# Optimization experiments

Hardware: AMD Instinct MI355X
Metric: run time of the kernel (lower is better)

Reference implementation:

```python
import jax, jax.numpy as jnp
import numpy as np

N, E, G, T = 4096, 16384, 128, 100
DIMS = [(5, 64), (64, 128), (128, 256)]
EPS = 1e-5


def setup_inputs() -> dict:
    key = jax.random.key(0)
    ks = iter(jax.random.split(key, 64))
    d = {}
    d["x"] = jax.random.normal(next(ks), (N, 5), jnp.float32)
    d["edge_index"] = jax.random.randint(next(ks), (2, E), 0, N, jnp.int64)
    d["edge_attr"] = jax.random.uniform(next(ks), (E, 3), jnp.float32)
    d["batch_seg"] = jnp.sort(jax.random.randint(next(ks), (N,), 0, G, jnp.int64))
    for l, (cin, cout) in enumerate(DIMS, start=1):
        d[f"l{l}_W1"] = jax.random.normal(next(ks), (3, 32), jnp.float32) * 0.3
        d[f"l{l}_b1"] = jnp.zeros((32,), jnp.float32)
        d[f"l{l}_W2"] = jax.random.normal(next(ks), (32, cin * cout), jnp.float32) * 0.05
        d[f"l{l}_b2"] = jnp.zeros((cin * cout,), jnp.float32)
        d[f"l{l}_root"] = jax.random.normal(next(ks), (cin, cout), jnp.float32) * 0.1
        d[f"l{l}_bias"] = jnp.zeros((cout,), jnp.float32)
        d[f"bn{l}_g"] = jnp.ones((cout,), jnp.float32)
        d[f"bn{l}_b"] = jnp.zeros((cout,), jnp.float32)
        d[f"bn{l}_m"] = jax.random.normal(next(ks), (cout,), jnp.float32) * 0.01
        d[f"bn{l}_v"] = jax.random.uniform(next(ks), (cout,), jnp.float32, 0.5, 1.5)
    d["mlp_W"] = jax.random.normal(next(ks), (256, T), jnp.float32) * 0.06
    d["mlp_b"] = jnp.zeros((T,), jnp.float32)
    return d


def _nnconv(h, src, dst, edge_attr, W1, b1, W2, b2, root, bias, cin, cout):
    # edge MLP -> per-edge weight matrix [E, cin, cout]
    ew = (jax.nn.relu(edge_attr @ W1 + b1) @ W2 + b2).reshape(-1, cin, cout)
    msg = jnp.einsum('ei,eio->eo', h[src], ew)  # gather + per-edge matmul
    ssum = jax.ops.segment_sum(msg, dst, num_segments=N)
    cnt = jax.ops.segment_sum(jnp.ones((msg.shape[0],), msg.dtype), dst, num_segments=N)
    agg = ssum / jnp.maximum(cnt, 1.0)[:, None]  # scatter-mean
    return h @ root + agg + bias


def _bn(h, g, b, m, v):
    return g * (h - m) * jax.lax.rsqrt(v + EPS) + b


def reference(x, edge_index, edge_attr, batch_seg,
              l1_W1, l1_b1, l1_W2, l1_b2, l1_root, l1_bias, bn1_g, bn1_b, bn1_m, bn1_v,
              l2_W1, l2_b1, l2_W2, l2_b2, l2_root, l2_bias, bn2_g, bn2_b, bn2_m, bn2_v,
              l3_W1, l3_b1, l3_W2, l3_b2, l3_root, l3_bias, bn3_g, bn3_b, bn3_m, bn3_v,
              mlp_W, mlp_b):
    src, dst = edge_index[0], edge_index[1]
    h = _nnconv(x, src, dst, edge_attr, l1_W1, l1_b1, l1_W2, l1_b2, l1_root, l1_bias, 5, 64)
    h = jax.nn.relu(_bn(h, bn1_g, bn1_b, bn1_m, bn1_v))
    h = _nnconv(h, src, dst, edge_attr, l2_W1, l2_b1, l2_W2, l2_b2, l2_root, l2_bias, 64, 128)
    h = jax.nn.relu(_bn(h, bn2_g, bn2_b, bn2_m, bn2_v))
    h = _nnconv(h, src, dst, edge_attr, l3_W1, l3_b1, l3_W2, l3_b2, l3_root, l3_bias, 128, 256)
    h = jax.nn.relu(_bn(h, bn3_g, bn3_b, bn3_m, bn3_v))
    # global mean pool over graphs
    psum = jax.ops.segment_sum(h, batch_seg, num_segments=G)
    pcnt = jax.ops.segment_sum(jnp.ones((N,), h.dtype), batch_seg, num_segments=G)
    pooled = psum / jnp.maximum(pcnt, 1.0)[:, None]
    out = pooled @ mlp_W + mlp_b
    return jnp.where(out > 0, out, 0.1 * out)  # LeakyReLU(0.1)
```

## Files before the change

### kernel.cpp

```cpp
#include <hip/hip_runtime.h>
#include <cstdint>
#include <cstddef>

#define BN_EPS 1e-5f

typedef short bf16x8 __attribute__((ext_vector_type(8)));
typedef float f32x4  __attribute__((ext_vector_type(4)));
typedef unsigned short u16x8 __attribute__((ext_vector_type(8)));

__device__ __forceinline__ uint16_t f2bf_rte(float f) {
  uint32_t u = __float_as_uint(f);
  uint32_t r = u + 0x7fffu + ((u >> 16) & 1u);
  return (uint16_t)(r >> 16);
}
__device__ __forceinline__ float bf2f(uint16_t h) {
  return __uint_as_float(((uint32_t)h) << 16);
}
__device__ __forceinline__ void split_bf(float v, uint16_t& hi, uint16_t& lo) {
  hi = f2bf_rte(v);
  lo = f2bf_rte(v - bf2f(hi));
}

__global__ void hist_k(const int* __restrict__ dst, int* __restrict__ cnt, int E) {
  int e = blockIdx.x * blockDim.x + threadIdx.x;
  if (e < E) atomicAdd(&cnt[dst[e]], 1);
}

__global__ __launch_bounds__(1024) void scan_k(const int* __restrict__ cnt,
                                               int* __restrict__ offsets,
                                               int* __restrict__ cursor,
                                               int N, int total) {
  __shared__ int part[1024];
  int t = threadIdx.x;
  int a0 = cnt[4*t+0], a1 = cnt[4*t+1], a2 = cnt[4*t+2], a3 = cnt[4*t+3];
  part[t] = a0 + a1 + a2 + a3;
  __syncthreads();
  for (int off = 1; off < 1024; off <<= 1) {
    int v = (t >= off) ? part[t - off] : 0;
    __syncthreads();
    part[t] += v;
    __syncthreads();
  }
  int excl = (t == 0) ? 0 : part[t-1];
  int o0 = excl, o1 = o0 + a0, o2 = o1 + a1, o3 = o2 + a2;
  offsets[4*t+0] = o0; offsets[4*t+1] = o1; offsets[4*t+2] = o2; offsets[4*t+3] = o3;
  cursor [4*t+0] = o0; cursor [4*t+1] = o1; cursor [4*t+2] = o2; cursor [4*t+3] = o3;
  if (t == 0) offsets[N] = total;
}

__global__ void scatter_k(const int* __restrict__ dst, int* __restrict__ cursor,
                          int* __restrict__ csr, int E) {
  int e = blockIdx.x * blockDim.x + threadIdx.x;
  if (e < E) {
    int d = dst[e];
    int pos = atomicAdd(&cursor[d], 1);
    csr[pos] = e;
  }
}

__device__ __forceinline__ void w2pt_one(int idx, const float* W2, const float* b2,
                                         const float* root, uint16_t* Bhi, uint16_t* Blo,
                                         int cin, int cout, int Kpad) {
  int o  = idx / Kpad;
  int ki = idx - o * Kpad;
  float v = 0.f;
  if (ki < 34 * cin) {
    int k = ki / cin;
    int i = ki - k * cin;
    if (k < 32)       v = W2[(size_t)k * cin * cout + (size_t)i * cout + o];
    else if (k == 32) v = b2[(size_t)i * cout + o];
    else              v = root[(size_t)i * cout + o];
  }
  uint16_t hi, lo;
  split_bf(v, hi, lo);
  Bhi[idx] = hi;
  Blo[idx] = lo;
}

__global__ void build_W2pT_all_k(const float* W2a, const float* b2a, const float* roota,
                                 uint16_t* Bhia, uint16_t* Bloa,
                                 const float* W2b, const float* b2b, const float* rootb,
                                 uint16_t* Bhib, uint16_t* Blob,
                                 const float* W2c, const float* b2c, const float* rootc,
                                 uint16_t* Bhic, uint16_t* Bloc) {
  const int T1 = 64 * 192, T2 = 128 * 2176, T3 = 256 * 4352;
  int idx = blockIdx.x * blockDim.x + threadIdx.x;
  if (idx < T1) {
    w2pt_one(idx, W2a, b2a, roota, Bhia, Bloa, 5, 64, 192);
  } else if (idx < T1 + T2) {
    w2pt_one(idx - T1, W2b, b2b, rootb, Bhib, Blob, 64, 128, 2176);
  } else if (idx < T1 + T2 + T3) {
    w2pt_one(idx - T1 - T2, W2c, b2c, rootc, Bhic, Bloc, 128, 256, 4352);
  }
}

template<int CIN>
__global__ __launch_bounds__(256) void build_S_vec_k(const float* __restrict__ Craw,
                                                     const float* __restrict__ pbias,
                                                     const float* __restrict__ pg,
                                                     const float* __restrict__ pb,
                                                     const float* __restrict__ pm,
                                                     const float* __restrict__ pv,
                                                     const float* __restrict__ ea,
                                                     const float* __restrict__ W1,
                                                     const float* __restrict__ b1,
                                                     const int* __restrict__ src,
                                                     const int* __restrict__ csr,
                                                     const int* __restrict__ offsets,
                                                     uint16_t* __restrict__ Shi,
                                                     uint16_t* __restrict__ Slo,
                                                     int Kpad) {
  constexpr int CH = 8;
  constexpr int K1 = 33 * CIN;
  constexpr int NCH = K1 / 8;
  constexpr int NP = (NCH + 255) / 256;
  __shared__ float hs[CH][CIN];
  __shared__ float zs[CH][33];
  __shared__ int   es[CH];
  __shared__ float sA[CIN], tA[CIN];
  const int n = blockIdx.x;
  const int tid = threadIdx.x;
  if (tid < CIN) {
    float s = pg[tid] * rsqrtf(pv[tid] + BN_EPS);
    sA[tid] = s;
    tA[tid] = (pbias[tid] - pm[tid]) * s + pb[tid];
  }
  const int base = offsets[n];
  const int deg  = offsets[n+1] - base;
  const float scale = 1.f / fmaxf((float)deg, 1.f);
  float acc[NP][8];
#pragma unroll
  for (int p = 0; p < NP; p++)
#pragma unroll
    for (int j = 0; j < 8; j++) acc[p][j] = 0.f;

  for (int c0 = 0; c0 < deg; c0 += CH) {
    const int cc = min(CH, deg - c0);
    if (tid < cc) es[tid] = csr[base + c0 + tid];
    __syncthreads();
    for (int idx = tid; idx < cc * CIN; idx += 256) {
      int slot = idx / CIN, i = idx - slot * CIN;
      float raw = Craw[(size_t)src[es[slot]] * CIN + i];
      hs[slot][i] = fmaxf(raw * sA[i] + tA[i], 0.f);
    }
    for (int idx = tid; idx < cc * 33; idx += 256) {
      int slot = idx / 33, k = idx - slot * 33;
      float v;
      if (k == 32) v = 1.f;
      else {
        int e = es[slot];
        v = fmaxf(ea[e*3+0] * W1[k] + ea[e*3+1] * W1[32 + k] + ea[e*3+2] * W1[64 + k] + b1[k], 0.f);
      }
      zs[slot][k] = v;
    }
    __syncthreads();
#pragma unroll
    for (int p = 0; p < NP; p++) {
      int ch = p * 256 + tid;
      if (ch < NCH) {
        int ki0 = ch * 8;
        int k  = ki0 / CIN;
        int i0 = ki0 & (CIN - 1);
        for (int c = 0; c < cc; c++) {
          float zv = zs[c][k];
          float4 h0 = *(const float4*)&hs[c][i0];
          float4 h1 = *(const float4*)&hs[c][i0 + 4];
          acc[p][0] += zv * h0.x; acc[p][1] += zv * h0.y;
          acc[p][2] += zv * h0.z; acc[p][3] += zv * h0.w;
          acc[p][4] += zv * h1.x; acc[p][5] += zv * h1.y;
          acc[p][6] += zv * h1.z; acc[p][7] += zv * h1.w;
        }
      }
    }
    __syncthreads();
  }
  const size_t rowb = (size_t)n * Kpad;
#pragma unroll
  for (int p = 0; p < NP; p++) {
    int ch = p * 256 + tid;
    if (ch < NCH) {
      u16x8 hv, lv;
#pragma unroll
      for (int j = 0; j < 8; j++) {
        uint16_t hi, lo;
        split_bf(acc[p][j] * scale, hi, lo);
        hv[j] = hi; lv[j] = lo;
      }
      *(u16x8*)(Shi + rowb + ch * 8) = hv;
      *(u16x8*)(Slo + rowb + ch * 8) = lv;
    }
  }
  __syncthreads();
  for (int c = tid; c < CIN / 8; c += 256) {
    int i0 = c * 8;
    u16x8 hv, lv;
#pragma unroll
    for (int j = 0; j < 8; j++) {
      int i = i0 + j;
      float raw = Craw[(size_t)n * CIN + i];
      float val = fmaxf(raw * sA[i] + tA[i], 0.f);
      uint16_t hi, lo;
      split_bf(val, hi, lo);
      hv[j] = hi; lv[j] = lo;
    }
    *(u16x8*)(Shi + rowb + K1 + i0) = hv;
    *(u16x8*)(Slo + rowb + K1 + i0) = lv;
  }
}

__global__ __launch_bounds__(256) void build_S5_k(const float* __restrict__ h,
                                                  const float* __restrict__ ea,
                                                  const float* __restrict__ W1,
                                                  const float* __restrict__ b1,
                                                  const int* __restrict__ src,
                                                  const int* __restrict__ csr,
                                                  const int* __restrict__ offsets,
                                                  uint16_t* __restrict__ Shi,
                                                  uint16_t* __restrict__ Slo,
                                                  int Kpad) {
  constexpr int CIN = 5, CH = 8;
  constexpr int K1 = 33 * CIN;
  constexpr int KT = 34 * CIN;
  __shared__ float hs[CH][CIN];
  __shared__ float zs[CH][33];
  __shared__ int   es[CH];
  const int n = blockIdx.x;
  const int tid = threadIdx.x;
  const int base = offsets[n];
  const int deg  = offsets[n+1] - base;
  const float scale = 1.f / fmaxf((float)deg, 1.f);
  float acc = 0.f;

  for (int c0 = 0; c0 < deg; c0 += CH) {
    const int cc = min(CH, deg - c0);
    if (tid < cc) es[tid] = csr[base + c0 + tid];
    __syncthreads();
    for (int idx = tid; idx < cc * CIN; idx += 256) {
      int slot = idx / CIN, i = idx - slot * CIN;
      hs[slot][i] = h[(size_t)src[es[slot]] * CIN + i];
    }
    for (int idx = tid; idx < cc * 33; idx += 256) {
      int slot = idx / 33, k = idx - slot * 33;
      float v;
      if (k == 32) v = 1.f;
      else {
        int e = es[slot];
        v = fmaxf(ea[e*3+0] * W1[k] + ea[e*3+1] * W1[32 + k] + ea[e*3+2] * W1[64 + k] + b1[k], 0.f);
      }
      zs[slot][k] = v;
    }
    __syncthreads();
    if (tid < K1) {
      int k = tid / CIN, i = tid - (tid / CIN) * CIN;
      float a = acc;
      for (int c = 0; c < cc; c++) a += zs[c][k] * hs[c][i];
      acc = a;
    }
    __syncthreads();
  }
  const size_t rowb = (size_t)n * Kpad;
  if (tid < K1) {
    uint16_t hi, lo;
    split_bf(acc * scale, hi, lo);
    Shi[rowb + tid] = hi;
    Slo[rowb + tid] = lo;
  }
  if (tid < CIN) {
    uint16_t hi, lo;
    split_bf(h[(size_t)n * CIN + tid], hi, lo);
    Shi[rowb + K1 + tid] = hi;
    Slo[rowb + K1 + tid] = lo;
  }
  for (int ki = KT + tid; ki < Kpad; ki += 256) {
    Shi[rowb + ki] = 0;
    Slo[rowb + ki] = 0;
  }
}

__global__ __launch_bounds__(512, 4) void mfma_gemm_at_k(const uint16_t* __restrict__ Ahi,
                                                         const uint16_t* __restrict__ Alo,
                                                         const uint16_t* __restrict__ Bhi,
                                                         const uint16_t* __restrict__ Blo,
                                                         float* __restrict__ C,
                                                         int Kpad, int Ncol,
                                                         int iters, int SK) {
  __shared__ uint16_t As[2][128][64];
  __shared__ uint16_t Bs[2][128][64];
  const int m0 = blockIdx.x * 128, n0 = blockIdx.y * 128;
  const int z  = blockIdx.z;
  const int ibase = iters / SK, irem = iters % SK;
  const int i0    = z * ibase + min(z, irem);
  const int niter = ibase + (z < irem ? 1 : 0);
  const int tid  = threadIdx.x;
  const int lane = tid & 63;
  const int wave = tid >> 6;
  const int wm = wave & 1;
  const int wn = wave >> 1;
  const int q  = lane >> 4;
  const int mr = lane & 15;

  f32x4 acc[4][2];
#pragma unroll
  for (int a = 0; a < 4; a++)
#pragma unroll
    for (int b = 0; b < 2; b++) acc[a][b] = (f32x4)0.f;

  for (int it = 0; it < niter; it++) {
    const int k0 = (i0 + it) * 64;
#pragma unroll
    for (int i = 0; i < 8; i++) {
      int chunk = i * 512 + tid;
      int coct = chunk & 7;
      int row  = (chunk >> 3) & 127;
      int plane = (chunk >> 10) & 1;
      int arr   = chunk >> 11;
      const uint16_t* gsrc = arr ? (plane ? Blo : Bhi) : (plane ? Alo : Ahi);
      int grow = (arr ? n0 : m0) + row;
      uint4 v = {0u, 0u, 0u, 0u};
      if (arr == 0 || grow < Ncol)
        v = *(const uint4*)(gsrc + (size_t)grow * Kpad + k0 + coct * 8);
      int soct = coct ^ (row & 7);
      uint16_t* ldst = arr ? &Bs[plane][row][soct * 8] : &As[plane][row][soct * 8];
      *(uint4*)ldst = v;
    }
    __syncthreads();
#pragma unroll
    for (int ks = 0; ks < 2; ks++) {
      const int oct = (ks * 4 + q) ^ (mr & 7);
      bf16x8 bh[2], bl[2];
#pragma unroll
      for (int fn = 0; fn < 2; fn++) {
        int row = wn * 32 + fn * 16 + mr;
        bh[fn] = *(const bf16x8*)&Bs[0][row][oct * 8];
        bl[fn] = *(const bf16x8*)&Bs[1][row][oct * 8];
      }
#pragma unroll
      for (int fm = 0; fm < 4; fm++) {
        int row = wm * 64 + fm * 16 + mr;
        bf16x8 ah = *(const bf16x8*)&As[0][row][oct * 8];
        bf16x8 al = *(const bf16x8*)&As[1][row][oct * 8];
#pragma unroll
        for (int fn = 0; fn < 2; fn++) {
          acc[fm][fn] = __builtin_amdgcn_mfma_f32_16x16x32_bf16(ah, bh[fn], acc[fm][fn], 0, 0, 0);
          acc[fm][fn] = __builtin_amdgcn_mfma_f32_16x16x32_bf16(ah, bl[fn], acc[fm][fn], 0, 0, 0);
          acc[fm][fn] = __builtin_amdgcn_mfma_f32_16x16x32_bf16(al, bh[fn], acc[fm][fn], 0, 0, 0);
        }
      }
    }
    __syncthreads();
  }

#pragma unroll
  for (int fm = 0; fm < 4; fm++) {
#pragma unroll
    for (int reg = 0; reg < 4; reg++) {
      int row = m0 + wm * 64 + fm * 16 + q * 4 + reg;
#pragma unroll
      for (int fn = 0; fn < 2; fn++) {
        int col = n0 + wn * 32 + fn * 16 + mr;
        if (col < Ncol)
          atomicAdd(&C[(size_t)row * Ncol + col], acc[fm][fn][reg]);
      }
    }
  }
}

__global__ __launch_bounds__(256) void pool_final_k(const float* __restrict__ Craw,
                                                    const float* __restrict__ pbias,
                                                    const float* __restrict__ pg,
                                                    const float* __restrict__ pb,
                                                    const float* __restrict__ pm,
                                                    const float* __restrict__ pv,
                                                    const int* __restrict__ seg,
                                                    const float* __restrict__ W,
                                                    const float* __restrict__ b,
                                                    float* __restrict__ out,
                                                    int N, int T) {
  __shared__ float pooled[256];
  const int g = blockIdx.x, tid = threadIdx.x;
  float s3 = pg[tid] * rsqrtf(pv[tid] + BN_EPS);
  float t3 = (pbias[tid] - pm[tid]) * s3 + pb[tid];
  int lo = 0, hi = N;
  while (lo < hi) { int mid = (lo + hi) >> 1; if (seg[mid] < g) lo = mid + 1; else hi = mid; }
  int lo2 = lo, hi2 = N;
  while (lo2 < hi2) { int mid = (lo2 + hi2) >> 1; if (seg[mid] < g + 1) lo2 = mid + 1; else hi2 = mid; }
  const int cnt = lo2 - lo;
  const float inv = 1.f / fmaxf((float)cnt, 1.f);
  float s = 0.f;
  for (int n = lo; n < lo2; n++)
    s += fmaxf(Craw[(size_t)n * 256 + tid] * s3 + t3, 0.f);
  pooled[tid] = s * inv;
  __syncthreads();
  if (tid < T) {
    float acc = b[tid];
    for (int o = 0; o < 256; o++) acc += pooled[o] * W[(size_t)o * T + tid];
    out[(size_t)g * T + tid] = (acc > 0.f) ? acc : 0.1f * acc;
  }
}

extern "C" void kernel_launch(void* const* d_in, const int* in_sizes, int n_in,
                              void* d_out, int out_size, void* d_ws, size_t ws_size,
                              hipStream_t stream) {
  const float* x   = (const float*)d_in[0];
  const int*   ei  = (const int*)d_in[1];
  const float* ea  = (const float*)d_in[2];
  const int*   seg = (const int*)d_in[3];

  const int N = in_sizes[0] / 5;
  const int E = in_sizes[2] / 3;
  const int T = in_sizes[35];
  const int G = out_size / T;
  const int* src = ei;
  const int* dst = ei + E;

  const float *W1[3], *b1[3], *W2[3], *b2[3], *root[3], *bias[3];
  const float *bng[3], *bnb[3], *bnm[3], *bnv[3];
  for (int l = 0; l < 3; l++) {
    int base = 4 + l * 10;
    W1[l]   = (const float*)d_in[base + 0];
    b1[l]   = (const float*)d_in[base + 1];
    W2[l]   = (const float*)d_in[base + 2];
    b2[l]   = (const float*)d_in[base + 3];
    root[l] = (const float*)d_in[base + 4];
    bias[l] = (const float*)d_in[base + 5];
    bng[l]  = (const float*)d_in[base + 6];
    bnb[l]  = (const float*)d_in[base + 7];
    bnm[l]  = (const float*)d_in[base + 8];
    bnv[l]  = (const float*)d_in[base + 9];
  }
  const float* mlpW = (const float*)d_in[34];
  const float* mlpb = (const float*)d_in[35];

  char* p = (char*)d_ws;
  auto carve = [&](size_t bytes) -> char* {
    char* r = p;
    p += (bytes + 255) & ~(size_t)255;
    return r;
  };
  char*  zbase = p;
  int*   cnt = (int*)carve((size_t)N * 4);
  float* C1  = (float*)carve((size_t)N * 64 * 4);
  float* C2  = (float*)carve((size_t)N * 128 * 4);
  float* C3  = (float*)carve((size_t)N * 256 * 4);
  size_t zbytes = (size_t)(p - zbase);

  int*      offsets = (int*)carve((size_t)(N + 1) * 4);
  int*      cursor  = (int*)carve((size_t)N * 4);
  int*      csr     = (int*)carve((size_t)E * 4);
  uint16_t* W1hi = (uint16_t*)carve((size_t)64 * 192 * 2);
  uint16_t* W1lo = (uint16_t*)carve((size_t)64 * 192 * 2);
  uint16_t* W2hi = (uint16_t*)carve((size_t)128 * 2176 * 2);
  uint16_t* W2lo = (uint16_t*)carve((size_t)128 * 2176 * 2);
  uint16_t* W3hi = (uint16_t*)carve((size_t)256 * 4352 * 2);
  uint16_t* W3lo = (uint16_t*)carve((size_t)256 * 4352 * 2);
  const int KPADMAX = 4352;
  uint16_t* Shi = (uint16_t*)carve((size_t)N * KPADMAX * 2);
  uint16_t* Slo = (uint16_t*)carve((size_t)N * KPADMAX * 2);

  hipMemsetAsync(zbase, 0, zbytes, stream);

  {
    int total = 64 * 192 + 128 * 2176 + 256 * 4352;
    build_W2pT_all_k<<<(total + 255) / 256, 256, 0, stream>>>(
        W2[0], b2[0], root[0], W1hi, W1lo,
        W2[1], b2[1], root[1], W2hi, W2lo,
        W2[2], b2[2], root[2], W3hi, W3lo);
  }

  hist_k<<<(E + 255) / 256, 256, 0, stream>>>(dst, cnt, E);
  scan_k<<<1, 1024, 0, stream>>>(cnt, offsets, cursor, N, E);
  scatter_k<<<(E + 255) / 256, 256, 0, stream>>>(dst, cursor, csr, E);

  build_S5_k<<<N, 256, 0, stream>>>(x, ea, W1[0], b1[0], src, csr, offsets, Shi, Slo, 192);
  {
    dim3 grid(N / 128, 1, 3);
    mfma_gemm_at_k<<<grid, 512, 0, stream>>>(Shi, Slo, W1hi, W1lo, C1, 192, 64, 3, 3);
  }
  build_S_vec_k<64><<<N, 256, 0, stream>>>(C1, bias[0], bng[0], bnb[0], bnm[0], bnv[0],
                                           ea, W1[1], b1[1], src, csr, offsets, Shi, Slo, 2176);
  {
    dim3 grid(N / 128, 1, 16);
    mfma_gemm_at_k<<<grid, 512, 0, stream>>>(Shi, Slo, W2hi, W2lo, C2, 2176, 128, 34, 16);
  }
  build_S_vec_k<128><<<N, 256, 0, stream>>>(C2, bias[1], bng[1], bnb[1], bnm[1], bnv[1],
                                            ea, W1[2], b1[2], src, csr, offsets, Shi, Slo, 4352);
  {
    dim3 grid(N / 128, 2, 8);
    mfma_gemm_at_k<<<grid, 512, 0, stream>>>(Shi, Slo, W3hi, W3lo, C3, 4352, 256, 68, 8);
  }

  pool_final_k<<<G, 256, 0, stream>>>(C3, bias[2], bng[2], bnb[2], bnm[2], bnv[2],
                                      seg, mlpW, mlpb, (float*)d_out, N, T);
}
```

Before: 311.3 us.

## Load GEMM tiles directly into LDS and fuse CSR build into one kernel

The split-bf16 GEMM is rewritten to use global_load_lds direct-to-LDS transfers, with each of 4 waves loading one plane (Ahi/Alo/Bhi/Blo). K-steps shrink to 32, and each wave computes a 64x64 output subtile with 16 accumulators. This is meant to cut register staging and VALU work during tile loads and to raise MFMA work per LDS read. The cost is fewer threads per block, more sync points per unit of K, and higher register pressure. Separately, the histogram, scan and scatter kernels are merged into one single-block kernel that uses LDS atomics, removing two launches and the global count and cursor buffers.

```diff
diff --git a/kernel.cpp b/kernel.cpp
--- a/kernel.cpp
+++ b/kernel.cpp
@@ -21,18 +21,24 @@
   lo = f2bf_rte(v - bf2f(hi));
 }
 
-__global__ void hist_k(const int* __restrict__ dst, int* __restrict__ cnt, int E) {
-  int e = blockIdx.x * blockDim.x + threadIdx.x;
-  if (e < E) atomicAdd(&cnt[dst[e]], 1);
-}
-
-__global__ __launch_bounds__(1024) void scan_k(const int* __restrict__ cnt,
-                                               int* __restrict__ offsets,
-                                               int* __restrict__ cursor,
-                                               int N, int total) {
+__device__ __forceinline__ void gl2lds16(const uint16_t* g, uint16_t* l) {
+  __builtin_amdgcn_global_load_lds(
+      (const __attribute__((address_space(1))) uint32_t*)g,
+      (__attribute__((address_space(3))) uint32_t*)l, 16, 0, 0);
+}
+
+__global__ __launch_bounds__(1024) void csr_build_k(const int* __restrict__ dst,
+                                                    int* __restrict__ offsets,
+                                                    int* __restrict__ csr,
+                                                    int N, int E) {
+  __shared__ int scnt[4096];
   __shared__ int part[1024];
-  int t = threadIdx.x;
-  int a0 = cnt[4*t+0], a1 = cnt[4*t+1], a2 = cnt[4*t+2], a3 = cnt[4*t+3];
+  const int t = threadIdx.x;
+  for (int i = t; i < N; i += 1024) scnt[i] = 0;
+  __syncthreads();
+  for (int e = t; e < E; e += 1024) atomicAdd(&scnt[dst[e]], 1);
+  __syncthreads();
+  int a0 = scnt[4*t+0], a1 = scnt[4*t+1], a2 = scnt[4*t+2], a3 = scnt[4*t+3];
   part[t] = a0 + a1 + a2 + a3;
   __syncthreads();
   for (int off = 1; off < 1024; off <<= 1) {
@@ -43,17 +49,13 @@
   }
   int excl = (t == 0) ? 0 : part[t-1];
   int o0 = excl, o1 = o0 + a0, o2 = o1 + a1, o3 = o2 + a2;
+  __syncthreads();
+  scnt[4*t+0] = o0; scnt[4*t+1] = o1; scnt[4*t+2] = o2; scnt[4*t+3] = o3;
   offsets[4*t+0] = o0; offsets[4*t+1] = o1; offsets[4*t+2] = o2; offsets[4*t+3] = o3;
-  cursor [4*t+0] = o0; cursor [4*t+1] = o1; cursor [4*t+2] = o2; cursor [4*t+3] = o3;
-  if (t == 0) offsets[N] = total;
-}
-
-__global__ void scatter_k(const int* __restrict__ dst, int* __restrict__ cursor,
-                          int* __restrict__ csr, int E) {
-  int e = blockIdx.x * blockDim.x + threadIdx.x;
-  if (e < E) {
-    int d = dst[e];
-    int pos = atomicAdd(&cursor[d], 1);
+  if (t == 0) offsets[N] = E;
+  __syncthreads();
+  for (int e = t; e < E; e += 1024) {
+    int pos = atomicAdd(&scnt[dst[e]], 1);
     csr[pos] = e;
   }
 }
@@ -277,15 +279,14 @@
   }
 }
 
-__global__ __launch_bounds__(512, 4) void mfma_gemm_at_k(const uint16_t* __restrict__ Ahi,
+__global__ __launch_bounds__(256, 3) void mfma_gemm_gl_k(const uint16_t* __restrict__ Ahi,
                                                          const uint16_t* __restrict__ Alo,
                                                          const uint16_t* __restrict__ Bhi,
                                                          const uint16_t* __restrict__ Blo,
                                                          float* __restrict__ C,
                                                          int Kpad, int Ncol,
                                                          int iters, int SK) {
-  __shared__ uint16_t As[2][128][64];
-  __shared__ uint16_t Bs[2][128][64];
+  __shared__ uint16_t lds[4][128][32];
   const int m0 = blockIdx.x * 128, n0 = blockIdx.y * 128;
   const int z  = blockIdx.z;
   const int ibase = iters / SK, irem = iters % SK;
@@ -294,53 +295,50 @@
   const int tid  = threadIdx.x;
   const int lane = tid & 63;
   const int wave = tid >> 6;
-  const int wm = wave & 1;
-  const int wn = wave >> 1;
+  const int wm = wave & 1, wn = wave >> 1;
   const int q  = lane >> 4;
   const int mr = lane & 15;
 
-  f32x4 acc[4][2];
+  const uint16_t* gplane = (wave == 0) ? Ahi : (wave == 1) ? Alo : (wave == 2) ? Bhi : Blo;
+  const int growbase = (wave < 2) ? m0 : n0;
+  const int rowclamp = (wave < 2) ? 0x7fffffff : (Ncol - 1);
+  const int lrow = lane >> 2;
+  const int loct = lane & 3;
+
+  f32x4 acc[4][4];
 #pragma unroll
   for (int a = 0; a < 4; a++)
 #pragma unroll
-    for (int b = 0; b < 2; b++) acc[a][b] = (f32x4)0.f;
+    for (int b = 0; b < 4; b++) acc[a][b] = (f32x4)0.f;
+
+  const int swz = (mr >> 1) & 3;
+  const int ol  = q ^ swz;
 
   for (int it = 0; it < niter; it++) {
-    const int k0 = (i0 + it) * 64;
+    const int k0 = (i0 + it) * 32;
 #pragma unroll
     for (int i = 0; i < 8; i++) {
-      int chunk = i * 512 + tid;
-      int coct = chunk & 7;
-      int row  = (chunk >> 3) & 127;
-      int plane = (chunk >> 10) & 1;
-      int arr   = chunk >> 11;
-      const uint16_t* gsrc = arr ? (plane ? Blo : Bhi) : (plane ? Alo : Ahi);
-      int grow = (arr ? n0 : m0) + row;
-      uint4 v = {0u, 0u, 0u, 0u};
-      if (arr == 0 || grow < Ncol)
-        v = *(const uint4*)(gsrc + (size_t)grow * Kpad + k0 + coct * 8);
-      int soct = coct ^ (row & 7);
-      uint16_t* ldst = arr ? &Bs[plane][row][soct * 8] : &As[plane][row][soct * 8];
-      *(uint4*)ldst = v;
-    }
-    __syncthreads();
-#pragma unroll
-    for (int ks = 0; ks < 2; ks++) {
-      const int oct = (ks * 4 + q) ^ (mr & 7);
-      bf16x8 bh[2], bl[2];
-#pragma unroll
-      for (int fn = 0; fn < 2; fn++) {
-        int row = wn * 32 + fn * 16 + mr;
-        bh[fn] = *(const bf16x8*)&Bs[0][row][oct * 8];
-        bl[fn] = *(const bf16x8*)&Bs[1][row][oct * 8];
+      int row = i * 16 + lrow;
+      int og  = loct ^ ((row >> 1) & 3);
+      int grow = min(growbase + row, rowclamp);
+      gl2lds16(gplane + (size_t)grow * Kpad + k0 + og * 8, &lds[wave][i * 16][0]);
+    }
+    __syncthreads();
+    {
+      bf16x8 bh[4], bl[4];
+#pragma unroll
+      for (int fn = 0; fn < 4; fn++) {
+        int r = wn * 64 + fn * 16 + mr;
+        bh[fn] = *(const bf16x8*)&lds[2][r][ol * 8];
+        bl[fn] = *(const bf16x8*)&lds[3][r][ol * 8];
       }
 #pragma unroll
       for (int fm = 0; fm < 4; fm++) {
-        int row = wm * 64 + fm * 16 + mr;
-        bf16x8 ah = *(const bf16x8*)&As[0][row][oct * 8];
-        bf16x8 al = *(const bf16x8*)&As[1][row][oct * 8];
-#pragma unroll
-        for (int fn = 0; fn < 2; fn++) {
+        int r = wm * 64 + fm * 16 + mr;
+        bf16x8 ah = *(const bf16x8*)&lds[0][r][ol * 8];
+        bf16x8 al = *(const bf16x8*)&lds[1][r][ol * 8];
+#pragma unroll
+        for (int fn = 0; fn < 4; fn++) {
           acc[fm][fn] = __builtin_amdgcn_mfma_f32_16x16x32_bf16(ah, bh[fn], acc[fm][fn], 0, 0, 0);
           acc[fm][fn] = __builtin_amdgcn_mfma_f32_16x16x32_bf16(ah, bl[fn], acc[fm][fn], 0, 0, 0);
           acc[fm][fn] = __builtin_amdgcn_mfma_f32_16x16x32_bf16(al, bh[fn], acc[fm][fn], 0, 0, 0);
@@ -356,8 +354,8 @@
     for (int reg = 0; reg < 4; reg++) {
       int row = m0 + wm * 64 + fm * 16 + q * 4 + reg;
 #pragma unroll
-      for (int fn = 0; fn < 2; fn++) {
-        int col = n0 + wn * 32 + fn * 16 + mr;
+      for (int fn = 0; fn < 4; fn++) {
+        int col = n0 + wn * 64 + fn * 16 + mr;
         if (col < Ncol)
           atomicAdd(&C[(size_t)row * Ncol + col], acc[fm][fn][reg]);
       }
@@ -438,14 +436,12 @@
     return r;
   };
   char*  zbase = p;
-  int*   cnt = (int*)carve((size_t)N * 4);
   float* C1  = (float*)carve((size_t)N * 64 * 4);
   float* C2  = (float*)carve((size_t)N * 128 * 4);
   float* C3  = (float*)carve((size_t)N * 256 * 4);
   size_t zbytes = (size_t)(p - zbase);
 
   int*      offsets = (int*)carve((size_t)(N + 1) * 4);
-  int*      cursor  = (int*)carve((size_t)N * 4);
   int*      csr     = (int*)carve((size_t)E * 4);
   uint16_t* W1hi = (uint16_t*)carve((size_t)64 * 192 * 2);
   uint16_t* W1lo = (uint16_t*)carve((size_t)64 * 192 * 2);
@@ -467,26 +463,24 @@
         W2[2], b2[2], root[2], W3hi, W3lo);
   }
 
-  hist_k<<<(E + 255) / 256, 256, 0, stream>>>(dst, cnt, E);
-  scan_k<<<1, 1024, 0, stream>>>(cnt, offsets, cursor, N, E);
-  scatter_k<<<(E + 255) / 256, 256, 0, stream>>>(dst, cursor, csr, E);
+  csr_build_k<<<1, 1024, 0, stream>>>(dst, offsets, csr, N, E);
 
   build_S5_k<<<N, 256, 0, stream>>>(x, ea, W1[0], b1[0], src, csr, offsets, Shi, Slo, 192);
   {
     dim3 grid(N / 128, 1, 3);
-    mfma_gemm_at_k<<<grid, 512, 0, stream>>>(Shi, Slo, W1hi, W1lo, C1, 192, 64, 3, 3);
+    mfma_gemm_gl_k<<<grid, 256, 0, stream>>>(Shi, Slo, W1hi, W1lo, C1, 192, 64, 6, 3);
   }
   build_S_vec_k<64><<<N, 256, 0, stream>>>(C1, bias[0], bng[0], bnb[0], bnm[0], bnv[0],
                                            ea, W1[1], b1[1], src, csr, offsets, Shi, Slo, 2176);
   {
     dim3 grid(N / 128, 1, 16);
-    mfma_gemm_at_k<<<grid, 512, 0, stream>>>(Shi, Slo, W2hi, W2lo, C2, 2176, 128, 34, 16);
+    mfma_gemm_gl_k<<<grid, 256, 0, stream>>>(Shi, Slo, W2hi, W2lo, C2, 2176, 128, 68, 16);
   }
   build_S_vec_k<128><<<N, 256, 0, stream>>>(C2, bias[1], bng[1], bnb[1], bnm[1], bnv[1],
                                             ea, W1[2], b1[2], src, csr, offsets, Shi, Slo, 4352);
   {
     dim3 grid(N / 128, 2, 8);
-    mfma_gemm_at_k<<<grid, 512, 0, stream>>>(Shi, Slo, W3hi, W3lo, C3, 4352, 256, 68, 8);
+    mfma_gemm_gl_k<<<grid, 256, 0, stream>>>(Shi, Slo, W3hi, W3lo, C3, 4352, 256, 136, 8);
   }
 
   pool_final_k<<<G, 256, 0, stream>>>(C3, bias[2], bng[2], bnb[2], bnm[2], bnv[2],
```

Measured after the change: 316.3 us. No clear change (+1.6%).
